# Kernel optimization log

Hardware: AMD Instinct MI355X
Metric: run time of the kernel (lower is better)

The kernel has to match this reference:

```python
import jax, jax.numpy as jnp
import numpy as np

N = 30000   # nodes
E = 300000  # edges
B = 64      # graphs
H = 4       # heads
C = 64      # channels per head
HC = H * C  # 256


def setup_inputs() -> dict:
    key = jax.random.key(0)
    ks = jax.random.split(key, 32)

    def rn(k, shape):
        scale = 1.0 / np.sqrt(shape[0])
        return (jax.random.normal(k, shape) * scale).astype(jnp.float32)

    inp = {}
    inp["x"] = jax.random.normal(ks[0], (N, 13), dtype=jnp.float32)
    inp["edge_index"] = jax.random.randint(ks[1], (2, E), 0, N, dtype=jnp.int64)
    inp["edge_attr"] = jax.random.normal(ks[2], (E, 51), dtype=jnp.float32)
    inp["batch"] = jnp.sort(jax.random.randint(ks[3], (N,), 0, B, dtype=jnp.int64))
    # init node MLP: Linear(13 -> 128) (plain_last => no act/norm)
    inp["W0"] = rn(ks[4], (13, 128)); inp["b0"] = jnp.zeros((128,), jnp.float32)
    # GATv2 layer 1: in 128 -> H=4, C=64
    inp["Wl1"] = rn(ks[5], (128, HC)); inp["bl1"] = jnp.zeros((HC,), jnp.float32)
    inp["Wr1"] = rn(ks[6], (128, HC)); inp["br1"] = jnp.zeros((HC,), jnp.float32)
    inp["We1"] = rn(ks[7], (51, HC))
    inp["att1"] = rn(ks[8], (H, C))
    inp["bias1"] = jnp.zeros((HC,), jnp.float32)
    # GATv2 layer 2: in 256 -> H=4, C=64
    inp["Wl2"] = rn(ks[9], (HC, HC)); inp["bl2"] = jnp.zeros((HC,), jnp.float32)
    inp["Wr2"] = rn(ks[10], (HC, HC)); inp["br2"] = jnp.zeros((HC,), jnp.float32)
    inp["We2"] = rn(ks[11], (51, HC))
    inp["att2"] = rn(ks[12], (H, C))
    inp["bias2"] = jnp.zeros((HC,), jnp.float32)
    # attention pooling MLP: Linear(256 -> 256) (plain_last)
    inp["Wp"] = rn(ks[13], (HC, HC)); inp["bp"] = jnp.zeros((HC,), jnp.float32)
    # out MLP: Linear(256->256)+BN+ReLU, Linear(256->2001)
    inp["Wo1"] = rn(ks[14], (HC, 256)); inp["bo1"] = jnp.zeros((256,), jnp.float32)
    inp["gamma"] = jnp.ones((256,), jnp.float32); inp["beta"] = jnp.zeros((256,), jnp.float32)
    inp["Wo2"] = rn(ks[15], (256, 2001)); inp["bo2"] = jnp.zeros((2001,), jnp.float32)
    return inp


def _gatv2(x, src, dst, ea, Wl, bl, Wr, br, We, att, bias):
    n = x.shape[0]
    xl = (x @ Wl + bl).reshape(n, H, C)   # source transform (also message content)
    xr = (x @ Wr + br).reshape(n, H, C)   # target transform
    ee = (ea @ We).reshape(-1, H, C)      # edge embedding, no bias
    z = jax.nn.leaky_relu(xl[src] + xr[dst] + ee, negative_slope=0.2)  # [E,H,C]
    logit = jnp.einsum('ehc,hc->eh', z, att)                           # [E,H]
    m = jax.ops.segment_max(logit, dst, num_segments=n)                # [N,H]
    w = jnp.exp(logit - m[dst])
    den = jax.ops.segment_sum(w, dst, num_segments=n)
    alpha = w / (den[dst] + 1e-16)                                     # segment softmax
    out = jax.ops.segment_sum(xl[src] * alpha[:, :, None], dst, num_segments=n)
    return out.reshape(n, HC) + bias


def _forward(x, edge_index, edge_attr, batch, W0, b0, Wl1, bl1, Wr1, br1, We1, att1, bias1,
             Wl2, bl2, Wr2, br2, We2, att2, bias2, Wp, bp, Wo1, bo1, gamma, beta, Wo2, bo2):
    src, dst = edge_index[0], edge_index[1]
    h = x @ W0 + b0
    h = _gatv2(h, src, dst, edge_attr, Wl1, bl1, Wr1, br1, We1, att1, bias1)
    h = _gatv2(h, src, dst, edge_attr, Wl2, bl2, Wr2, br2, We2, att2, bias2)
    # softmax attention pooling over nodes of each graph (per feature column)
    a = h @ Wp + bp                                       # [N,HC]
    am = jax.ops.segment_max(a, batch, num_segments=B)
    aw = jnp.exp(a - am[batch])
    ad = jax.ops.segment_sum(aw, batch, num_segments=B)
    attw = aw / (ad[batch] + 1e-16)
    g = jax.ops.segment_sum(h * attw, batch, num_segments=B)  # [B,HC]
    # out MLP: Linear + BatchNorm(train stats) + ReLU + Linear, then leaky_relu
    y = g @ Wo1 + bo1
    mu = jnp.mean(y, axis=0)
    var = jnp.var(y, axis=0)
    y = (y - mu) / jnp.sqrt(var + 1e-5) * gamma + beta
    y = jax.nn.relu(y)
    y = y @ Wo2 + bo2
    return jax.nn.leaky_relu(y, negative_slope=0.01)


def reference(x, edge_index, edge_attr, batch, W0, b0, Wl1, bl1, Wr1, br1, We1, att1, bias1,
              Wl2, bl2, Wr2, br2, We2, att2, bias2, Wp, bp, Wo1, bo1, gamma, beta, Wo2, bo2):
    return _forward(x, edge_index, edge_attr, batch, W0, b0, Wl1, bl1, Wr1, br1, We1, att1, bias1,
                    Wl2, bl2, Wr2, br2, We2, att2, bias2, Wp, bp, Wo1, bo1, gamma, beta, Wo2, bo2)
```

## Files before the change

### kernel.cpp

```cpp
#include <hip/hip_runtime.h>
#include <hip/hip_bf16.h>

#define NN 30000
#define EE 300000
#define BB 64
#define HH 4
#define CC 64
#define HC 256

typedef __attribute__((ext_vector_type(8))) short short8;
typedef __attribute__((ext_vector_type(4))) float floatx4;

__device__ __forceinline__ float b2f(short x) {
    return __uint_as_float(((unsigned)(unsigned short)x) << 16);
}
__device__ __forceinline__ unsigned short f2b(float f) {
    __hip_bfloat16 h = __float2bfloat16(f);
    return *(unsigned short*)&h;
}

#define GLD16(gp, lp) __builtin_amdgcn_global_load_lds( \
    (const __attribute__((address_space(1))) void*)(gp), \
    (__attribute__((address_space(3))) void*)(lp), 16, 0, 0)

#define ROT2(x) ((((x) << 2) | ((x) >> 3)) & 31)
#define EESWZ(chunk, row) (ROT2(chunk) ^ (((row) >> 2) & 3) ^ (((row) & 1) << 2))

template<int CT>
__global__ __launch_bounds__(256) void mfma_gemm(
    const ushort* __restrict__ A, const ushort* __restrict__ Bt,
    const float* __restrict__ bias, float* __restrict__ outF,
    __hip_bfloat16* __restrict__ outB, int M, int Nc, int K) {
    constexpr int SMEM_USHORTS =
        ((64 * 32 + CT * 64 * 32) > (64 * CT * 64)) ? (64 * 32 + CT * 64 * 32)
                                                    : (64 * CT * 64);
    __shared__ __align__(16) ushort smem[SMEM_USHORTS];
    ushort* lA = smem;
    ushort* lB = smem + 64 * 32;
    const int tid = threadIdx.x, lane = tid & 63, wv = tid >> 6;
    const int row0 = blockIdx.x * 64, col0 = blockIdx.y * (CT * 64);

    floatx4 acc[4][CT];
#pragma unroll
    for (int r = 0; r < 4; r++)
#pragma unroll
        for (int c = 0; c < CT; c++) acc[r][c] = (floatx4){0.f, 0.f, 0.f, 0.f};

    const int arow = tid >> 2;
    const int sl   = (tid & 3) ^ ((tid >> 3) & 3);
    const ushort* ga = A + (size_t)(row0 + arow) * K + sl * 8;
    const int m16 = lane & 15, q = lane >> 4;

    for (int k0 = 0; k0 < K; k0 += 32) {
        __syncthreads();
        GLD16(ga + k0, &lA[tid * 8]);
#pragma unroll
        for (int j = 0; j < CT; j++) {
            const ushort* gb = Bt + (size_t)(col0 + j * 64 + arow) * K + k0 + sl * 8;
            GLD16(gb, &lB[j * 2048 + tid * 8]);
        }
        __syncthreads();
        short8 aF[4], bF[CT];
#pragma unroll
        for (int r = 0; r < 4; r++) {
            int rr = r * 16 + m16;
            aF[r] = *(const short8*)&lA[rr * 32 + ((q ^ ((rr >> 1) & 3)) << 3)];
        }
#pragma unroll
        for (int c = 0; c < CT; c++) {
            int nr = (wv * CT + c) * 16 + m16;
            bF[c] = *(const short8*)&lB[nr * 32 + ((q ^ ((nr >> 1) & 3)) << 3)];
        }
#pragma unroll
        for (int r = 0; r < 4; r++)
#pragma unroll
            for (int c = 0; c < CT; c++)
                acc[r][c] = __builtin_amdgcn_mfma_f32_16x16x32_bf16(aF[r], bF[c], acc[r][c], 0, 0, 0);
    }

    if (outB != nullptr) {
        __syncthreads();
#pragma unroll
        for (int c = 0; c < CT; c++) {
            int lcol = (wv * CT + c) * 16 + m16;
            float bv = bias ? bias[col0 + lcol] : 0.f;
            int ch = lcol >> 3, c7 = lcol & 7;
#pragma unroll
            for (int r = 0; r < 4; r++)
#pragma unroll
                for (int j = 0; j < 4; j++) {
                    int row = r * 16 + q * 4 + j;
                    smem[row * (CT * 64) + ((ch ^ (row & 7)) << 3) + c7] =
                        f2b(acc[r][c][j] + bv);
                }
        }
        __syncthreads();
        constexpr int SH = (CT == 4) ? 5 : 4;
#pragma unroll
        for (int s = 0; s < CT * 2; s++) {
            int g = tid + 256 * s;
            int row = g >> SH, ch = g & (CT * 8 - 1);
            int grow = row0 + row;
            if (grow < M) {
                short8 v = *(const short8*)&smem[row * (CT * 64) + ((ch ^ (row & 7)) << 3)];
                *(short8*)((ushort*)outB + (size_t)grow * Nc + col0 + ch * 8) = v;
            }
        }
    } else {
#pragma unroll
        for (int c = 0; c < CT; c++) {
            int col = col0 + (wv * CT + c) * 16 + m16;
            float bv = bias ? bias[col] : 0.f;
#pragma unroll
            for (int r = 0; r < 4; r++)
#pragma unroll
                for (int j = 0; j < 4; j++) {
                    int row = row0 + r * 16 + q * 4 + j;
                    if (row < M) outF[(size_t)row * Nc + col] = acc[r][c][j] + bv;
                }
        }
    }
}

__global__ void permute_ea_frag(const float* __restrict__ ea,
                                const int* __restrict__ einv,
                                ushort* __restrict__ ea_frag) {
    const int t = blockIdx.x * 256 + threadIdx.x;
    const int e = t >> 3, ch = t & 7;
    if (e >= 300032) return;
    const bool live = e < EE;
    const int p = live ? einv[e] : e;
    short8 v8;
#pragma unroll
    for (int j = 0; j < 8; j++) {
        int k = ch * 8 + j;
        float v = (live && k < 51) ? ea[(size_t)e * 51 + k] : 0.f;
        v8[j] = (short)f2b(v);
    }
    *(short8*)&ea_frag[(size_t)p * 64 + ch * 8] = v8;
}

struct SetupParams {
    const float *x, *W0, *Wl1, *Wr1, *Wl2, *Wr2, *Wp, *We1, *We2;
    const float *bl1, *br1, *bl2, *br2;
    __hip_bfloat16 *xpad, *W0t, *W1t, *W2t, *Wpt;
    ushort *Wef1, *Wef2;
    float *bcat1, *bcat2;
    int *deg;
};
__global__ void setup_all(SetupParams P) {
    const int b = blockIdx.x, t = threadIdx.x;
    if (b < 3750) {
        int i = b * 256 + t;
        if (i < NN) P.deg[i] = 0;
        int n = i >> 5, k = i & 31;
        P.xpad[i] = __float2bfloat16(k < 13 ? P.x[n * 13 + k] : 0.f);
    } else if (b < 3766) {
        int o = (b - 3750) * 256 + t;
        int n = o >> 5, k = o & 31;
        P.W0t[o] = __float2bfloat16(k < 13 ? P.W0[k * 128 + n] : 0.f);
    } else if (b < 3894) {
        int o = (b - 3766) * 256 + t;
        int n = o >> 7, k = o & 127;
        P.W1t[(size_t)n * 128 + k] = __float2bfloat16(P.Wl1[k * 256 + n]);
    } else if (b < 4022) {
        int o = (b - 3894) * 256 + t;
        int n = o >> 7, k = o & 127;
        P.W1t[(size_t)(256 + n) * 128 + k] = __float2bfloat16(P.Wr1[k * 256 + n]);
    } else if (b < 4278) {
        int o = (b - 4022) * 256 + t;
        int n = o >> 8, k = o & 255;
        P.W2t[(size_t)n * 256 + k] = __float2bfloat16(P.Wl2[k * 256 + n]);
    } else if (b < 4534) {
        int o = (b - 4278) * 256 + t;
        int n = o >> 8, k = o & 255;
        P.W2t[(size_t)(256 + n) * 256 + k] = __float2bfloat16(P.Wr2[k * 256 + n]);
    } else if (b < 4790) {
        int o = (b - 4534) * 256 + t;
        int n = o >> 8, k = o & 255;
        P.Wpt[(size_t)n * 256 + k] = __float2bfloat16(P.Wp[k * 256 + n]);
    } else if (b < 4918) {
        int which = (b - 4790) >> 6;
        int o = ((b - 4790) & 63) * 256 + t;
        const float* We = which ? P.We2 : P.We1;
        ushort* Wf = which ? P.Wef2 : P.Wef1;
        int j = o & 7, m16 = (o >> 3) & 15, ch = (o >> 7) & 7, nt = o >> 10;
        int n = nt * 16 + m16, k = ch * 8 + j;
        Wf[o] = f2b(k < 51 ? We[k * 256 + n] : 0.f);
    } else {
        int i = (b - 4918) * 256 + t;
        int pair = i >> 9, idx = i & 511;
        const float* a = pair ? P.bl2 : P.bl1;
        const float* bb = pair ? P.br2 : P.br1;
        float* o = pair ? P.bcat2 : P.bcat1;
        o[idx] = idx < 256 ? a[idx] : bb[idx - 256];
    }
}

__global__ __launch_bounds__(256, 4) void edge_fused(
    const ushort* __restrict__ ea_frag, const ushort* __restrict__ Wfrag,
    const float* __restrict__ att,
    const int* __restrict__ src_csr, const int* __restrict__ dst_csr,
    const ushort* __restrict__ xlr, float* __restrict__ logitp) {
    __shared__ __align__(16) ushort eeS[64 * 256];
    __shared__ float satt[4 * 72];
    const int tid = threadIdx.x, lane = tid & 63, wv = tid >> 6;
    const int tile = ((int)blockIdx.x & 7) * 586 + ((int)blockIdx.x >> 3);
    const int i0 = tile * 64;
    satt[(tid >> 6) * 72 + (tid & 63)] = att[tid];
    const int m16 = lane & 15, q = lane >> 4;

    const int el = tid >> 2, h = tid & 3;
    const int i = i0 + el;
    const bool live_e = (i < EE);
    const int ic = live_e ? i : (EE - 1);
    const int src = src_csr[ic], dstn = dst_csr[ic];
    const ushort* xlp = xlr + (size_t)src * 512 + h * 64;
    short8 xlv[8];
#pragma unroll
    for (int c = 0; c < 8; c++) xlv[c] = *(const short8*)(xlp + c * 8);

    const ushort* gtile = ea_frag + (size_t)i0 * 64;
    GLD16(gtile + tid * 8, &eeS[tid * 8]);
    GLD16(gtile + 2048 + tid * 8, &eeS[2048 + tid * 8]);
    __syncthreads();

    short8 zz;
#pragma unroll
    for (int z = 0; z < 8; z++) zz[z] = 0;

    short8 aF[2][4];
#pragma unroll
    for (int k0 = 0; k0 < 2; k0++)
#pragma unroll
        for (int r = 0; r < 4; r++)
            aF[k0][r] = (k0 == 1 && q == 3)
                ? zz
                : *(const short8*)&eeS[(r * 16 + m16) * 64 + (k0 * 4 + q) * 8];
    __syncthreads();

#pragma unroll
    for (int h2 = 0; h2 < 2; h2++) {
        floatx4 acc[4][2];
#pragma unroll
        for (int r = 0; r < 4; r++)
#pragma unroll
            for (int c = 0; c < 2; c++) acc[r][c] = (floatx4){0.f, 0.f, 0.f, 0.f};
#pragma unroll
        for (int k0 = 0; k0 < 2; k0++) {
            const bool live = !(k0 == 1 && q == 3);
            short8 bF[2];
#pragma unroll
            for (int c = 0; c < 2; c++)
                bF[c] = live
                    ? *(const short8*)&Wfrag[(((wv * 4 + h2 * 2 + c) * 8 + k0 * 4 + q) * 16 + m16) * 8]
                    : zz;
#pragma unroll
            for (int r = 0; r < 4; r++)
#pragma unroll
                for (int c = 0; c < 2; c++)
                    acc[r][c] = __builtin_amdgcn_mfma_f32_16x16x32_bf16(
                        aF[k0][r], bF[c], acc[r][c], 0, 0, 0);
        }
#pragma unroll
        for (int r = 0; r < 4; r++)
#pragma unroll
            for (int cc = 0; cc < 2; cc++)
#pragma unroll
                for (int j = 0; j < 4; j++) {
                    int row = r * 16 + q * 4 + j;
                    int col = (wv * 4 + h2 * 2 + cc) * 16 + m16;
                    int chunk = col >> 3;
                    int P = EESWZ(chunk, row);
                    eeS[row * 256 + (P << 3) + (col & 7)] = f2b(acc[r][cc][j]);
                }
        __builtin_amdgcn_sched_barrier(0);
    }
    __syncthreads();

    if (live_e) {
        const ushort* xrp = xlr + (size_t)dstn * 512 + 256 + h * 64;
        float s = 0.f;
#pragma unroll
        for (int c = 0; c < 8; c++) {
            short8 xrv = *(const short8*)(xrp + c * 8);
            int chunk = h * 8 + c;
            int P = EESWZ(chunk, el);
            short8 eev = *(const short8*)&eeS[el * 256 + (P << 3)];
#pragma unroll
            for (int j = 0; j < 8; j++) {
                float v = b2f(xlv[c][j]) + b2f(xrv[j]) + b2f(eev[j]);
                v = v > 0.f ? v : 0.2f * v;
                s += v * satt[h * 72 + c * 8 + j];
            }
        }
        logitp[(size_t)i * 4 + h] = s;
    }
}

__global__ void hist_deg(const int* __restrict__ ei, int* __restrict__ deg,
                         unsigned* __restrict__ am) {
    int e = blockIdx.x * 256 + threadIdx.x;
    if (e < BB * HC) am[e] = 0u;
    if (e < EE) atomicAdd(&deg[ei[EE + e]], 1);
}
__global__ void scan1(const int* __restrict__ deg, int* __restrict__ partial,
                      int* __restrict__ bsum) {
    __shared__ int sh[256];
    int t = threadIdx.x, i = blockIdx.x * 256 + t;
    int v = (i < NN) ? deg[i] : 0;
    sh[t] = v; __syncthreads();
    for (int off = 1; off < 256; off <<= 1) {
        int x = (t >= off) ? sh[t - off] : 0;
        __syncthreads();
        sh[t] += x;
        __syncthreads();
    }
    if (i < NN) partial[i] = sh[t] - v;
    if (t == 255) bsum[blockIdx.x] = sh[255];
}
__global__ void scan2(int* __restrict__ bsum, int nb) {
    __shared__ int sh[256];
    int t = threadIdx.x;
    int v = (t < nb) ? bsum[t] : 0;
    sh[t] = v; __syncthreads();
    for (int off = 1; off < 256; off <<= 1) {
        int x = (t >= off) ? sh[t - off] : 0;
        __syncthreads();
        sh[t] += x;
        __syncthreads();
    }
    if (t < nb) bsum[t] = sh[t] - v;
}
__global__ void scan3(const int* __restrict__ partial, const int* __restrict__ bsum,
                      int* __restrict__ start, int* __restrict__ cursor) {
    int i = blockIdx.x * 256 + threadIdx.x;
    if (i < NN) { start[i] = partial[i] + bsum[i >> 8]; cursor[i] = 0; }
    else if (i == NN) start[NN] = EE;
}
__global__ void scatter_e(const int* __restrict__ ei, int* __restrict__ cursor,
                          const int* __restrict__ start, int* __restrict__ einv,
                          int* __restrict__ src_csr, int* __restrict__ dst_csr) {
    int e = blockIdx.x * 256 + threadIdx.x;
    if (e >= EE) return;
    int s = ei[e];
    int d = ei[EE + e];
    int p = atomicAdd(&cursor[d], 1);
    int pos = start[d] + p;
    einv[e] = pos;
    src_csr[pos] = s;
    dst_csr[pos] = d;
}

__global__ __launch_bounds__(256) void aggregate_csr(
    const ushort* __restrict__ xlr, const float* __restrict__ logitp,
    const int* __restrict__ src_csr, const int* __restrict__ start,
    const float* __restrict__ bias, ushort* __restrict__ outb) {
    const int lane = threadIdx.x & 63, wv = threadIdx.x >> 6;
    const int g = ((int)blockIdx.x & 7) * 938 + ((int)blockIdx.x >> 3);
    if (g >= (NN + 3) / 4) return;
    const int dst = g * 4 + wv;
    if (dst >= NN) return;
    const int s0 = start[dst];
    const int deg = start[dst + 1] - s0;
    const int h = lane >> 4;

    float m[4] = {-3.4e38f, -3.4e38f, -3.4e38f, -3.4e38f};
    float lg[4] = {0.f, 0.f, 0.f, 0.f};
    bool lv = lane < deg;
    if (lv) {
        float4 l4 = ((const float4*)logitp)[s0 + lane];
        lg[0] = l4.x; lg[1] = l4.y; lg[2] = l4.z; lg[3] = l4.w;
        m[0] = l4.x; m[1] = l4.y; m[2] = l4.z; m[3] = l4.w;
    }
    for (int i = 64 + lane; i < deg; i += 64) {
        float4 l4 = ((const float4*)logitp)[s0 + i];
        m[0] = fmaxf(m[0], l4.x); m[1] = fmaxf(m[1], l4.y);
        m[2] = fmaxf(m[2], l4.z); m[3] = fmaxf(m[3], l4.w);
    }
#pragma unroll
    for (int off = 32; off; off >>= 1)
#pragma unroll
        for (int k = 0; k < 4; k++) m[k] = fmaxf(m[k], __shfl_xor(m[k], off));

    float d[4];
#pragma unroll
    for (int k = 0; k < 4; k++) d[k] = lv ? __expf(lg[k] - m[k]) : 0.f;
    for (int i = 64 + lane; i < deg; i += 64) {
        float4 l4 = ((const float4*)logitp)[s0 + i];
        d[0] += __expf(l4.x - m[0]); d[1] += __expf(l4.y - m[1]);
        d[2] += __expf(l4.z - m[2]); d[3] += __expf(l4.w - m[3]);
    }
#pragma unroll
    for (int off = 32; off; off >>= 1)
#pragma unroll
        for (int k = 0; k < 4; k++) d[k] += __shfl_xor(d[k], off);
    const float dh = 1.f / (((h == 0) ? d[0] : (h == 1) ? d[1] : (h == 2) ? d[2] : d[3]) + 1e-16f);
    const float mh = (h == 0) ? m[0] : (h == 1) ? m[1] : (h == 2) ? m[2] : m[3];

    float4 b4 = ((const float4*)bias)[lane];
    float a0 = b4.x, a1 = b4.y, a2 = b4.z, a3 = b4.w;

    const ushort* xbase = xlr + (size_t)lane * 4;
    const float* lgh = logitp + h;
    int i = 0;
    for (; i + 8 <= deg; i += 8) {
        int sv[8]; float aw[8];
#pragma unroll
        for (int u = 0; u < 8; u++) {
            sv[u] = src_csr[s0 + i + u];
            float lh = lgh[(size_t)(s0 + i + u) * 4];
            aw[u] = __expf(lh - mh) * dh;
        }
        ushort4 xv[8];
#pragma unroll
        for (int u = 0; u < 8; u++)
            xv[u] = *(const ushort4*)(xbase + (size_t)sv[u] * 512);
#pragma unroll
        for (int u = 0; u < 8; u++) {
            a0 += b2f(xv[u].x) * aw[u]; a1 += b2f(xv[u].y) * aw[u];
            a2 += b2f(xv[u].z) * aw[u]; a3 += b2f(xv[u].w) * aw[u];
        }
    }
    for (; i < deg; i++) {
        int srcv = src_csr[s0 + i];
        float lh = lgh[(size_t)(s0 + i) * 4];
        float aw = __expf(lh - mh) * dh;
        ushort4 xv = *(const ushort4*)(xbase + (size_t)srcv * 512);
        a0 += b2f(xv.x) * aw; a1 += b2f(xv.y) * aw;
        a2 += b2f(xv.z) * aw; a3 += b2f(xv.w) * aw;
    }
    ushort4 ov;
    ov.x = f2b(a0); ov.y = f2b(a1); ov.z = f2b(a2); ov.w = f2b(a3);
    *(ushort4*)(outb + (size_t)dst * 256 + lane * 4) = ov;
}

__device__ __forceinline__ unsigned fmap(float f) {
    unsigned u = __float_as_uint(f);
    return (u & 0x80000000u) ? ~u : (u | 0x80000000u);
}
__device__ __forceinline__ float funmap(unsigned u) {
    return (u & 0x80000000u) ? __uint_as_float(u & 0x7FFFFFFFu)
                             : __uint_as_float(~u);
}

__global__ void pool_max(const __hip_bfloat16* __restrict__ a, const int* __restrict__ batch,
                         unsigned* __restrict__ am, float* __restrict__ den,
                         float* __restrict__ num) {
    const int c = threadIdx.x;
    if (blockIdx.x < BB) {
        den[blockIdx.x * HC + c] = 0.f;
        num[blockIdx.x * HC + c] = 0.f;
    }
    const int n0 = blockIdx.x * 64;
    int curb = batch[n0];
    float m = -3.4e38f;
    const int nend = min(n0 + 64, NN);
    for (int n = n0; n < nend; n++) {
        int b = batch[n];
        float v = __bfloat162float(a[(size_t)n * HC + c]);
        if (b != curb) { atomicMax(&am[curb * HC + c], fmap(m)); curb = b; m = v; }
        else           { m = fmaxf(m, v); }
    }
    atomicMax(&am[curb * HC + c], fmap(m));
}
__global__ void pool_sums(const __hip_bfloat16* __restrict__ a,
                          const __hip_bfloat16* __restrict__ h2,
                          const int* __restrict__ batch, const unsigned* __restrict__ am,
                          float* __restrict__ den, float* __restrict__ num) {
    const int c = threadIdx.x;
    const int n0 = blockIdx.x * 64;
    int curb = batch[n0];
    float sd = 0.f, sn = 0.f;
    float mcur = funmap(am[curb * HC + c]);
    const int nend = min(n0 + 64, NN);
    for (int n = n0; n < nend; n++) {
        int b = batch[n];
        if (b != curb) {
            atomicAdd(&den[curb * HC + c], sd);
            atomicAdd(&num[curb * HC + c], sn);
            curb = b; sd = 0.f; sn = 0.f; mcur = funmap(am[b * HC + c]);
        }
        float w = __expf(__bfloat162float(a[(size_t)n * HC + c]) - mcur);
        sd += w;
        sn += __bfloat162float(h2[(size_t)n * HC + c]) * w;
    }
    atomicAdd(&den[curb * HC + c], sd);
    atomicAdd(&num[curb * HC + c], sn);
}

__global__ void mlp_lin1(const float* __restrict__ num, const float* __restrict__ den,
                         const float* __restrict__ Wo1, const float* __restrict__ bo1,
                         float* __restrict__ y) {
    __shared__ float gsh[HC];
    const int c = threadIdx.x;
    const int r = blockIdx.x;
    gsh[c] = num[r * HC + c] / (den[r * HC + c] + 1e-16f);
    __syncthreads();
    float acc = bo1[c];
#pragma unroll 4
    for (int k = 0; k < HC; k++) acc = fmaf(gsh[k], Wo1[k * HC + c], acc);
    y[r * HC + c] = acc;
}
__global__ void bn_lin2(const float* __restrict__ y, const float* __restrict__ gamma,
                        const float* __restrict__ beta, const float* __restrict__ Wo2,
                        const float* __restrict__ bo2, float* __restrict__ out) {
    __shared__ float ysh[HC];
    const int t = threadIdx.x;
    const int r = blockIdx.y;
    float s = 0.f, sq = 0.f;
    for (int rr = 0; rr < BB; rr++) { float v = y[rr * HC + t]; s += v; sq += v * v; }
    float mu  = s * (1.f / BB);
    float var = sq * (1.f / BB) - mu * mu;
    float inv = rsqrtf(var + 1e-5f) * gamma[t];
    float v = (y[r * HC + t] - mu) * inv + beta[t];
    ysh[t] = v > 0.f ? v : 0.f;
    __syncthreads();
    int j = blockIdx.x * 256 + t;
    if (j >= 2001) return;
    float acc = bo2[j];
#pragma unroll 4
    for (int k = 0; k < HC; k++) acc = fmaf(ysh[k], Wo2[k * 2001 + j], acc);
    out[r * 2001 + j] = acc > 0.f ? acc : 0.01f * acc;
}

extern "C" void kernel_launch(void* const* d_in, const int* in_sizes, int n_in,
                              void* d_out, int out_size, void* d_ws, size_t ws_size,
                              hipStream_t stream) {
    const float* x     = (const float*)d_in[0];
    const int*   ei    = (const int*)d_in[1];
    const float* ea    = (const float*)d_in[2];
    const int*   batch = (const int*)d_in[3];
    const float* W0 = (const float*)d_in[4];  const float* b0 = (const float*)d_in[5];
    const float* Wl1 = (const float*)d_in[6]; const float* bl1 = (const float*)d_in[7];
    const float* Wr1 = (const float*)d_in[8]; const float* br1 = (const float*)d_in[9];
    const float* We1 = (const float*)d_in[10]; const float* att1 = (const float*)d_in[11];
    const float* bias1 = (const float*)d_in[12];
    const float* Wl2 = (const float*)d_in[13]; const float* bl2 = (const float*)d_in[14];
    const float* Wr2 = (const float*)d_in[15]; const float* br2 = (const float*)d_in[16];
    const float* We2 = (const float*)d_in[17]; const float* att2 = (const float*)d_in[18];
    const float* bias2 = (const float*)d_in[19];
    const float* Wp = (const float*)d_in[20]; const float* bp = (const float*)d_in[21];
    const float* Wo1 = (const float*)d_in[22]; const float* bo1 = (const float*)d_in[23];
    const float* gamma = (const float*)d_in[24]; const float* beta = (const float*)d_in[25];
    const float* Wo2 = (const float*)d_in[26]; const float* bo2 = (const float*)d_in[27];
    float* out = (float*)d_out;

    char* p = (char*)d_ws;
    auto alloc = [&](size_t bytes) { char* r = p; p += (bytes + 255) & ~(size_t)255; return r; };
    const int MP = 30016;
    const int ET = 4688;
    __hip_bfloat16* xpad  = (__hip_bfloat16*)alloc((size_t)MP * 32 * 2);
    __hip_bfloat16* W0t   = (__hip_bfloat16*)alloc(128 * 32 * 2);
    __hip_bfloat16* W1t   = (__hip_bfloat16*)alloc(512 * 128 * 2);
    __hip_bfloat16* W2t   = (__hip_bfloat16*)alloc(512 * 256 * 2);
    __hip_bfloat16* Wpt   = (__hip_bfloat16*)alloc(256 * 256 * 2);
    ushort* Wef1 = (ushort*)alloc(256 * 64 * 2);
    ushort* Wef2 = (ushort*)alloc(256 * 64 * 2);
    float* bcat1 = (float*)alloc(512 * 4);
    float* bcat2 = (float*)alloc(512 * 4);
    __hip_bfloat16* h0b  = (__hip_bfloat16*)alloc((size_t)MP * 128 * 2);
    __hip_bfloat16* xlrb = (__hip_bfloat16*)alloc((size_t)MP * 512 * 2);
    __hip_bfloat16* h1b  = (__hip_bfloat16*)alloc((size_t)MP * 256 * 2);
    __hip_bfloat16* h2b  = (__hip_bfloat16*)alloc((size_t)MP * 256 * 2);
    ushort* ea_frag = (ushort*)alloc((size_t)ET * 4096 * 2);
    __hip_bfloat16* abuf = (__hip_bfloat16*)alloc((size_t)MP * 256 * 2);
    float* logit = (float*)alloc((size_t)EE * 4 * 4);
    int* deg    = (int*)alloc(NN * 4);
    int* cursor = (int*)alloc(NN * 4);
    int* partial= (int*)alloc(NN * 4);
    int* bsum   = (int*)alloc(256 * 4);
    int* start  = (int*)alloc((NN + 4) * 4);
    int* einv   = (int*)alloc((size_t)EE * 4);
    int* src_csr= (int*)alloc((size_t)EE * 4);
    int* dst_csr= (int*)alloc((size_t)EE * 4);
    unsigned* am = (unsigned*)alloc(BB * HC * 4);
    float* den  = (float*)alloc(BB * HC * 4);
    float* num  = (float*)alloc(BB * HC * 4);
    float* ybuf = (float*)alloc(BB * HC * 4);

    const int NB = (NN + 255) / 256;

    SetupParams sp;
    sp.x = x; sp.W0 = W0; sp.Wl1 = Wl1; sp.Wr1 = Wr1; sp.Wl2 = Wl2; sp.Wr2 = Wr2;
    sp.Wp = Wp; sp.We1 = We1; sp.We2 = We2;
    sp.bl1 = bl1; sp.br1 = br1; sp.bl2 = bl2; sp.br2 = br2;
    sp.xpad = xpad; sp.W0t = W0t; sp.W1t = W1t; sp.W2t = W2t; sp.Wpt = Wpt;
    sp.Wef1 = Wef1; sp.Wef2 = Wef2; sp.bcat1 = bcat1; sp.bcat2 = bcat2;
    sp.deg = deg;
    setup_all<<<4922, 256, 0, stream>>>(sp);

    hist_deg<<<(EE + 255) / 256, 256, 0, stream>>>(ei, deg, am);
    scan1<<<NB, 256, 0, stream>>>(deg, partial, bsum);
    scan2<<<1, 256, 0, stream>>>(bsum, NB);
    scan3<<<NB + 1, 256, 0, stream>>>(partial, bsum, start, cursor);
    scatter_e<<<(EE + 255) / 256, 256, 0, stream>>>(ei, cursor, start, einv, src_csr, dst_csr);
    permute_ea_frag<<<9376, 256, 0, stream>>>(ea, einv, ea_frag);

    mfma_gemm<2><<<dim3(469, 1), 256, 0, stream>>>(
        (const ushort*)xpad, (const ushort*)W0t, b0, nullptr, h0b, NN, 128, 32);

    mfma_gemm<4><<<dim3(469, 2), 256, 0, stream>>>(
        (const ushort*)h0b, (const ushort*)W1t, bcat1, nullptr, xlrb, NN, 512, 128);
    edge_fused<<<ET, 256, 0, stream>>>(ea_frag, Wef1, att1, src_csr, dst_csr,
                                       (const ushort*)xlrb, logit);
    aggregate_csr<<<7504, 256, 0, stream>>>(
        (const ushort*)xlrb, logit, src_csr, start, bias1, (ushort*)h1b);

    mfma_gemm<4><<<dim3(469, 2), 256, 0, stream>>>(
        (const ushort*)h1b, (const ushort*)W2t, bcat2, nullptr, xlrb, NN, 512, 256);
    edge_fused<<<ET, 256, 0, stream>>>(ea_frag, Wef2, att2, src_csr, dst_csr,
                                       (const ushort*)xlrb, logit);
    aggregate_csr<<<7504, 256, 0, stream>>>(
        (const ushort*)xlrb, logit, src_csr, start, bias2, (ushort*)h2b);

    mfma_gemm<4><<<dim3(469, 1), 256, 0, stream>>>(
        (const ushort*)h2b, (const ushort*)Wpt, bp, nullptr, abuf, NN, 256, 256);
    const int poolGrid = (NN + 63) / 64;
    pool_max<<<poolGrid, HC, 0, stream>>>(abuf, batch, am, den, num);
    pool_sums<<<poolGrid, HC, 0, stream>>>(abuf, h2b, batch, am, den, num);

    mlp_lin1<<<BB, HC, 0, stream>>>(num, den, Wo1, bo1, ybuf);
    bn_lin2<<<dim3(8, BB), 256, 0, stream>>>(ybuf, gamma, beta, Wo2, bo2, out);
}
```

Measured before the change: 538.0 us.

## Fold init linear into layer-1 weights, merge scan kernels, fuse pooling per graph

Precomputes W0·[Wl1|Wr1] and the matching folded bias in the setup kernel, so layer 1 runs a single K=32 GEMM straight from padded x instead of two GEMMs through an intermediate h0 buffer. Merges scan2 into scan3 by having each block reduce the preceding block sums itself. Replaces the two-pass atomic pool_max/pool_sums with one kernel per (graph, column slice) that binary-searches the sorted batch array for its node range and does max then sums with no atomics. The trade-offs are a serial 128-step dot product per weight element in setup, a dependence on batch being sorted, and low parallelism in pooling (64x4 blocks each looping over about 470 nodes).

```diff
diff --git a/kernel.cpp b/kernel.cpp
--- a/kernel.cpp
+++ b/kernel.cpp
@@ -141,11 +141,11 @@
 }
 
 struct SetupParams {
-    const float *x, *W0, *Wl1, *Wr1, *Wl2, *Wr2, *Wp, *We1, *We2;
+    const float *x, *W0, *b0, *Wl1, *Wr1, *Wl2, *Wr2, *Wp, *We1, *We2;
     const float *bl1, *br1, *bl2, *br2;
-    __hip_bfloat16 *xpad, *W0t, *W1t, *W2t, *Wpt;
-    ushort *Wef1, *Wef2;
-    float *bcat1, *bcat2;
+    __hip_bfloat16 *xpad, *W2t, *Wpt;
+    ushort *Wef1, *Wef2, *Wct;
+    float *bcat2, *bc;
     int *deg;
 };
 __global__ void setup_all(SetupParams P) {
@@ -155,45 +155,45 @@
         if (i < NN) P.deg[i] = 0;
         int n = i >> 5, k = i & 31;
         P.xpad[i] = __float2bfloat16(k < 13 ? P.x[n * 13 + k] : 0.f);
-    } else if (b < 3766) {
+    } else if (b < 4006) {
         int o = (b - 3750) * 256 + t;
-        int n = o >> 5, k = o & 31;
-        P.W0t[o] = __float2bfloat16(k < 13 ? P.W0[k * 128 + n] : 0.f);
-    } else if (b < 3894) {
-        int o = (b - 3766) * 256 + t;
-        int n = o >> 7, k = o & 127;
-        P.W1t[(size_t)n * 128 + k] = __float2bfloat16(P.Wl1[k * 256 + n]);
-    } else if (b < 4022) {
-        int o = (b - 3894) * 256 + t;
-        int n = o >> 7, k = o & 127;
-        P.W1t[(size_t)(256 + n) * 128 + k] = __float2bfloat16(P.Wr1[k * 256 + n]);
-    } else if (b < 4278) {
-        int o = (b - 4022) * 256 + t;
         int n = o >> 8, k = o & 255;
         P.W2t[(size_t)n * 256 + k] = __float2bfloat16(P.Wl2[k * 256 + n]);
-    } else if (b < 4534) {
-        int o = (b - 4278) * 256 + t;
+    } else if (b < 4262) {
+        int o = (b - 4006) * 256 + t;
         int n = o >> 8, k = o & 255;
         P.W2t[(size_t)(256 + n) * 256 + k] = __float2bfloat16(P.Wr2[k * 256 + n]);
-    } else if (b < 4790) {
-        int o = (b - 4534) * 256 + t;
+    } else if (b < 4518) {
+        int o = (b - 4262) * 256 + t;
         int n = o >> 8, k = o & 255;
         P.Wpt[(size_t)n * 256 + k] = __float2bfloat16(P.Wp[k * 256 + n]);
-    } else if (b < 4918) {
-        int which = (b - 4790) >> 6;
-        int o = ((b - 4790) & 63) * 256 + t;
+    } else if (b < 4646) {
+        int which = (b - 4518) >> 6;
+        int o = ((b - 4518) & 63) * 256 + t;
         const float* We = which ? P.We2 : P.We1;
         ushort* Wf = which ? P.Wef2 : P.Wef1;
         int j = o & 7, m16 = (o >> 3) & 15, ch = (o >> 7) & 7, nt = o >> 10;
         int n = nt * 16 + m16, k = ch * 8 + j;
         Wf[o] = f2b(k < 51 ? We[k * 256 + n] : 0.f);
+    } else if (b < 4648) {
+        int idx = (b - 4646) * 256 + t;
+        P.bcat2[idx] = idx < 256 ? P.bl2[idx] : P.br2[idx - 256];
     } else {
-        int i = (b - 4918) * 256 + t;
-        int pair = i >> 9, idx = i & 511;
-        const float* a = pair ? P.bl2 : P.bl1;
-        const float* bb = pair ? P.br2 : P.br1;
-        float* o = pair ? P.bcat2 : P.bcat1;
-        o[idx] = idx < 256 ? a[idx] : bb[idx - 256];
+        int o = (b - 4648) * 256 + t;
+        int n = o >> 5, k = o & 31;
+        int nn = n & 255;
+        const float* Wc = (n < 256) ? P.Wl1 : P.Wr1;
+        float s = 0.f;
+        if (k < 13)
+            for (int m = 0; m < 128; m++)
+                s = fmaf(P.W0[k * 128 + m], Wc[m * 256 + nn], s);
+        P.Wct[n * 32 + k] = f2b(s);
+        if (k == 0) {
+            float bb = (n < 256) ? P.bl1[nn] : P.br1[nn];
+            for (int m = 0; m < 128; m++)
+                bb = fmaf(P.b0[m], Wc[m * 256 + nn], bb);
+            P.bc[n] = bb;
+        }
     }
 }
 
@@ -298,10 +298,8 @@
     }
 }
 
-__global__ void hist_deg(const int* __restrict__ ei, int* __restrict__ deg,
-                         unsigned* __restrict__ am) {
+__global__ void hist_deg(const int* __restrict__ ei, int* __restrict__ deg) {
     int e = blockIdx.x * 256 + threadIdx.x;
-    if (e < BB * HC) am[e] = 0u;
     if (e < EE) atomicAdd(&deg[ei[EE + e]], 1);
 }
 __global__ void scan1(const int* __restrict__ deg, int* __restrict__ partial,
@@ -319,23 +317,20 @@
     if (i < NN) partial[i] = sh[t] - v;
     if (t == 255) bsum[blockIdx.x] = sh[255];
 }
-__global__ void scan2(int* __restrict__ bsum, int nb) {
-    __shared__ int sh[256];
-    int t = threadIdx.x;
-    int v = (t < nb) ? bsum[t] : 0;
-    sh[t] = v; __syncthreads();
-    for (int off = 1; off < 256; off <<= 1) {
-        int x = (t >= off) ? sh[t - off] : 0;
-        __syncthreads();
-        sh[t] += x;
-        __syncthreads();
-    }
-    if (t < nb) bsum[t] = sh[t] - v;
-}
 __global__ void scan3(const int* __restrict__ partial, const int* __restrict__ bsum,
                       int* __restrict__ start, int* __restrict__ cursor) {
-    int i = blockIdx.x * 256 + threadIdx.x;
-    if (i < NN) { start[i] = partial[i] + bsum[i >> 8]; cursor[i] = 0; }
+    __shared__ int sh[256];
+    const int t = threadIdx.x;
+    const int myb = blockIdx.x;
+    int v = (t < myb && t < 118) ? bsum[t] : 0;
+    sh[t] = v; __syncthreads();
+    for (int off = 128; off; off >>= 1) {
+        if (t < off) sh[t] += sh[t + off];
+        __syncthreads();
+    }
+    const int pre = sh[0];
+    int i = myb * 256 + t;
+    if (i < NN) { start[i] = partial[i] + pre; cursor[i] = 0; }
     else if (i == NN) start[NN] = EE;
 }
 __global__ void scatter_e(const int* __restrict__ ei, int* __restrict__ cursor,
@@ -435,58 +430,36 @@
     *(ushort4*)(outb + (size_t)dst * 256 + lane * 4) = ov;
 }
 
-__device__ __forceinline__ unsigned fmap(float f) {
-    unsigned u = __float_as_uint(f);
-    return (u & 0x80000000u) ? ~u : (u | 0x80000000u);
-}
-__device__ __forceinline__ float funmap(unsigned u) {
-    return (u & 0x80000000u) ? __uint_as_float(u & 0x7FFFFFFFu)
-                             : __uint_as_float(~u);
-}
-
-__global__ void pool_max(const __hip_bfloat16* __restrict__ a, const int* __restrict__ batch,
-                         unsigned* __restrict__ am, float* __restrict__ den,
-                         float* __restrict__ num) {
-    const int c = threadIdx.x;
-    if (blockIdx.x < BB) {
-        den[blockIdx.x * HC + c] = 0.f;
-        num[blockIdx.x * HC + c] = 0.f;
-    }
-    const int n0 = blockIdx.x * 64;
-    int curb = batch[n0];
+__global__ void pool_fused(const __hip_bfloat16* __restrict__ a,
+                           const __hip_bfloat16* __restrict__ h2,
+                           const int* __restrict__ batch,
+                           float* __restrict__ den, float* __restrict__ num) {
+    const int b = blockIdx.x;
+    const int c = blockIdx.y * 64 + threadIdx.x;
+    __shared__ int s0s, s1s;
+    if (threadIdx.x == 0) {
+        int lo = 0, hi = NN;
+        while (lo < hi) { int mid = (lo + hi) >> 1; if (batch[mid] < b) lo = mid + 1; else hi = mid; }
+        s0s = lo;
+    }
+    if (threadIdx.x == 1) {
+        int lo = 0, hi = NN;
+        while (lo < hi) { int mid = (lo + hi) >> 1; if (batch[mid] < b + 1) lo = mid + 1; else hi = mid; }
+        s1s = lo;
+    }
+    __syncthreads();
+    const int n0 = s0s, n1 = s1s;
     float m = -3.4e38f;
-    const int nend = min(n0 + 64, NN);
-    for (int n = n0; n < nend; n++) {
-        int b = batch[n];
-        float v = __bfloat162float(a[(size_t)n * HC + c]);
-        if (b != curb) { atomicMax(&am[curb * HC + c], fmap(m)); curb = b; m = v; }
-        else           { m = fmaxf(m, v); }
-    }
-    atomicMax(&am[curb * HC + c], fmap(m));
-}
-__global__ void pool_sums(const __hip_bfloat16* __restrict__ a,
-                          const __hip_bfloat16* __restrict__ h2,
-                          const int* __restrict__ batch, const unsigned* __restrict__ am,
-                          float* __restrict__ den, float* __restrict__ num) {
-    const int c = threadIdx.x;
-    const int n0 = blockIdx.x * 64;
-    int curb = batch[n0];
+    for (int n = n0; n < n1; n++)
+        m = fmaxf(m, __bfloat162float(a[(size_t)n * HC + c]));
     float sd = 0.f, sn = 0.f;
-    float mcur = funmap(am[curb * HC + c]);
-    const int nend = min(n0 + 64, NN);
-    for (int n = n0; n < nend; n++) {
-        int b = batch[n];
-        if (b != curb) {
-            atomicAdd(&den[curb * HC + c], sd);
-            atomicAdd(&num[curb * HC + c], sn);
-            curb = b; sd = 0.f; sn = 0.f; mcur = funmap(am[b * HC + c]);
-        }
-        float w = __expf(__bfloat162float(a[(size_t)n * HC + c]) - mcur);
+    for (int n = n0; n < n1; n++) {
+        float w = __expf(__bfloat162float(a[(size_t)n * HC + c]) - m);
         sd += w;
         sn += __bfloat162float(h2[(size_t)n * HC + c]) * w;
     }
-    atomicAdd(&den[curb * HC + c], sd);
-    atomicAdd(&num[curb * HC + c], sn);
+    den[b * HC + c] = sd;
+    num[b * HC + c] = sn;
 }
 
 __global__ void mlp_lin1(const float* __restrict__ num, const float* __restrict__ den,
@@ -551,15 +524,13 @@
     const int MP = 30016;
     const int ET = 4688;
     __hip_bfloat16* xpad  = (__hip_bfloat16*)alloc((size_t)MP * 32 * 2);
-    __hip_bfloat16* W0t   = (__hip_bfloat16*)alloc(128 * 32 * 2);
-    __hip_bfloat16* W1t   = (__hip_bfloat16*)alloc(512 * 128 * 2);
     __hip_bfloat16* W2t   = (__hip_bfloat16*)alloc(512 * 256 * 2);
     __hip_bfloat16* Wpt   = (__hip_bfloat16*)alloc(256 * 256 * 2);
     ushort* Wef1 = (ushort*)alloc(256 * 64 * 2);
     ushort* Wef2 = (ushort*)alloc(256 * 64 * 2);
-    float* bcat1 = (float*)alloc(512 * 4);
+    ushort* Wct  = (ushort*)alloc(512 * 32 * 2);
+    float* bc    = (float*)alloc(512 * 4);
     float* bcat2 = (float*)alloc(512 * 4);
-    __hip_bfloat16* h0b  = (__hip_bfloat16*)alloc((size_t)MP * 128 * 2);
     __hip_bfloat16* xlrb = (__hip_bfloat16*)alloc((size_t)MP * 512 * 2);
     __hip_bfloat16* h1b  = (__hip_bfloat16*)alloc((size_t)MP * 256 * 2);
     __hip_bfloat16* h2b  = (__hip_bfloat16*)alloc((size_t)MP * 256 * 2);
@@ -574,7 +545,6 @@
     int* einv   = (int*)alloc((size_t)EE * 4);
     int* src_csr= (int*)alloc((size_t)EE * 4);
     int* dst_csr= (int*)alloc((size_t)EE * 4);
-    unsigned* am = (unsigned*)alloc(BB * HC * 4);
     float* den  = (float*)alloc(BB * HC * 4);
     float* num  = (float*)alloc(BB * HC * 4);
     float* ybuf = (float*)alloc(BB * HC * 4);
@@ -582,26 +552,22 @@
     const int NB = (NN + 255) / 256;
 
     SetupParams sp;
-    sp.x = x; sp.W0 = W0; sp.Wl1 = Wl1; sp.Wr1 = Wr1; sp.Wl2 = Wl2; sp.Wr2 = Wr2;
-    sp.Wp = Wp; sp.We1 = We1; sp.We2 = We2;
+    sp.x = x; sp.W0 = W0; sp.b0 = b0; sp.Wl1 = Wl1; sp.Wr1 = Wr1;
+    sp.Wl2 = Wl2; sp.Wr2 = Wr2; sp.Wp = Wp; sp.We1 = We1; sp.We2 = We2;
     sp.bl1 = bl1; sp.br1 = br1; sp.bl2 = bl2; sp.br2 = br2;
-    sp.xpad = xpad; sp.W0t = W0t; sp.W1t = W1t; sp.W2t = W2t; sp.Wpt = Wpt;
-    sp.Wef1 = Wef1; sp.Wef2 = Wef2; sp.bcat1 = bcat1; sp.bcat2 = bcat2;
-    sp.deg = deg;
-    setup_all<<<4922, 256, 0, stream>>>(sp);
-
-    hist_deg<<<(EE + 255) / 256, 256, 0, stream>>>(ei, deg, am);
+    sp.xpad = xpad; sp.W2t = W2t; sp.Wpt = Wpt;
+    sp.Wef1 = Wef1; sp.Wef2 = Wef2; sp.Wct = Wct;
+    sp.bcat2 = bcat2; sp.bc = bc; sp.deg = deg;
+    setup_all<<<4712, 256, 0, stream>>>(sp);
+
+    hist_deg<<<(EE + 255) / 256, 256, 0, stream>>>(ei, deg);
     scan1<<<NB, 256, 0, stream>>>(deg, partial, bsum);
-    scan2<<<1, 256, 0, stream>>>(bsum, NB);
     scan3<<<NB + 1, 256, 0, stream>>>(partial, bsum, start, cursor);
     scatter_e<<<(EE + 255) / 256, 256, 0, stream>>>(ei, cursor, start, einv, src_csr, dst_csr);
     permute_ea_frag<<<9376, 256, 0, stream>>>(ea, einv, ea_frag);
 
-    mfma_gemm<2><<<dim3(469, 1), 256, 0, stream>>>(
-        (const ushort*)xpad, (const ushort*)W0t, b0, nullptr, h0b, NN, 128, 32);
-
     mfma_gemm<4><<<dim3(469, 2), 256, 0, stream>>>(
-        (const ushort*)h0b, (const ushort*)W1t, bcat1, nullptr, xlrb, NN, 512, 128);
+        (const ushort*)xpad, Wct, bc, nullptr, xlrb, NN, 512, 32);
     edge_fused<<<ET, 256, 0, stream>>>(ea_frag, Wef1, att1, src_csr, dst_csr,
                                        (const ushort*)xlrb, logit);
     aggregate_csr<<<7504, 256, 0, stream>>>(
@@ -616,9 +582,7 @@
 
     mfma_gemm<4><<<dim3(469, 1), 256, 0, stream>>>(
         (const ushort*)h2b, (const ushort*)Wpt, bp, nullptr, abuf, NN, 256, 256);
-    const int poolGrid = (NN + 63) / 64;
-    pool_max<<<poolGrid, HC, 0, stream>>>(abuf, batch, am, den, num);
-    pool_sums<<<poolGrid, HC, 0, stream>>>(abuf, h2b, batch, am, den, num);
+    pool_fused<<<dim3(BB, 4), 64, 0, stream>>>(abuf, h2b, batch, den, num);
 
     mlp_lin1<<<BB, HC, 0, stream>>>(num, den, Wo1, bo1, ybuf);
     bn_lin2<<<dim3(8, BB), 256, 0, stream>>>(ybuf, gamma, beta, Wo2, bo2, out);
```

Result: slower. 698.6 us (+29.8%).
